# Optimization experiments

Measured on AMD Instinct MI355X. Metric: run time of the kernel, lower is better.

Reference implementation:

```python
import jax, jax.numpy as jnp
import numpy as np

B, S, D, H = 2, 2048, 1024, 16
HD = D // H  # head_dim = 64


def setup_inputs() -> dict:
    key = jax.random.key(0)
    ks = jax.random.split(key, 9)
    s = 1.0 / np.sqrt(D)
    return {
        "x": jax.random.normal(ks[0], (B, S, D), dtype=jnp.float32),
        "Wq": jax.random.uniform(ks[1], (D, D), jnp.float32, -s, s),
        "bq": jnp.zeros((D,), jnp.float32),
        "Wk": jax.random.uniform(ks[2], (D, D), jnp.float32, -s, s),
        "bk": jnp.zeros((D,), jnp.float32),
        "Wv": jax.random.uniform(ks[3], (D, D), jnp.float32, -s, s),
        "bv": jnp.zeros((D,), jnp.float32),
        "Wo": jax.random.uniform(ks[4], (D, D), jnp.float32, -s, s),
        "bo": jnp.zeros((D,), jnp.float32),
    }


def reference(x, Wq, bq, Wk, bk, Wv, bv, Wo, bo):
    # x: [B,S,D] -> Q/K/V: [B,H,S,HD]
    def heads(t):
        return t.reshape(B, S, H, HD).transpose(0, 2, 1, 3)

    Q = heads(x @ Wq + bq)
    K = heads(x @ Wk + bk)
    V = heads(x @ Wv + bv)
    scale = jnp.sqrt(jnp.asarray(HD, dtype=x.dtype))
    energy = jnp.einsum("bhqd,bhkd->bhqk", Q, K) / scale  # [B,H,S,S]
    attn = jax.nn.softmax(energy, axis=-1)
    # dropout is identity in eval mode
    o = jnp.einsum("bhqk,bhkd->bhqd", attn, V)  # [B,H,S,HD]
    o = o.transpose(0, 2, 1, 3).reshape(B, S, D)
    return o @ Wo + bo
```

## Files before the change

### kernel.cpp

```cpp
#include <hip/hip_runtime.h>
#include <hip/hip_bf16.h>

#define B_  2
#define S_  2048
#define D_  1024
#define H_  16
#define HD_ 64

typedef __attribute__((ext_vector_type(8))) short bf16x8;
typedef __attribute__((ext_vector_type(4))) float f32x4;

typedef __attribute__((address_space(1))) const short gbl_short;
typedef __attribute__((address_space(3))) short lds_short;

__device__ __forceinline__ short f2bf(float f) {
  union { float f; unsigned u; } v; v.f = f;
  unsigned r = (v.u + 0x7FFFu + ((v.u >> 16) & 1u)) >> 16;
  return (short)r;
}

__device__ __forceinline__ short bf16s(float f) {
  __hip_bfloat16 h = __float2bfloat16(f);
  return *reinterpret_cast<short*>(&h);
}

__global__ __launch_bounds__(256) void cast_x_kernel(const float* __restrict__ x,
                                                     short* __restrict__ xb) {
  int i = blockIdx.x * 256 + threadIdx.x;
  float4 v = ((const float4*)x)[i];
  short4 o;
  o.x = f2bf(v.x); o.y = f2bf(v.y); o.z = f2bf(v.z); o.w = f2bf(v.w);
  ((short4*)xb)[i] = o;
}

__global__ __launch_bounds__(256) void transpose_cast_w(
    const float* __restrict__ w0, const float* __restrict__ w1,
    const float* __restrict__ w2, const float* __restrict__ w3,
    short* __restrict__ t0, short* __restrict__ t1,
    short* __restrict__ t2, short* __restrict__ t3) {
  const float* W = blockIdx.z == 0 ? w0 : blockIdx.z == 1 ? w1 : blockIdx.z == 2 ? w2 : w3;
  short* T       = blockIdx.z == 0 ? t0 : blockIdx.z == 1 ? t1 : blockIdx.z == 2 ? t2 : t3;
  __shared__ float tile[32][33];
  int tx = threadIdx.x, ty = threadIdx.y;
  int x0 = blockIdx.x * 32, y0 = blockIdx.y * 32;
#pragma unroll
  for (int i = 0; i < 4; ++i)
    tile[ty + i * 8][tx] = W[(y0 + ty + i * 8) * D_ + x0 + tx];
  __syncthreads();
#pragma unroll
  for (int i = 0; i < 4; ++i)
    T[(x0 + ty + i * 8) * D_ + y0 + tx] = f2bf(tile[tx][ty + i * 8]);
}

__device__ __forceinline__ void gemm_mainloop(
    const short* __restrict__ A, const short* __restrict__ Bt, int K,
    int m0, int n0, short* lA, short* lB, f32x4 acc[4][4],
    int lane, int wave) {
  const int l15 = lane & 15, quad = lane >> 4;
  const int wm = wave & 1, wn = wave >> 1;
  const int srow = lane >> 2;
  const int skp  = (lane & 3) * 8;

  for (int kk = 0; kk < K; kk += 32) {
#pragma unroll
    for (int j = 0; j < 2; ++j) {
      int c = wave * 2 + j;
      int row = c * 16 + srow;
      __builtin_amdgcn_global_load_lds(
          (gbl_short*)(A + (m0 + row) * K + kk + skp),
          (lds_short*)(lA + c * 512 + lane * 8), 16, 0, 0);
      __builtin_amdgcn_global_load_lds(
          (gbl_short*)(Bt + (n0 + row) * K + kk + skp),
          (lds_short*)(lB + c * 512 + lane * 8), 16, 0, 0);
    }
    __syncthreads();

    bf16x8 af[4], bf[4];
#pragma unroll
    for (int i = 0; i < 4; ++i) {
      af[i] = *(const bf16x8*)(lA + (wm * 64 + i * 16 + l15) * 32 + quad * 8);
      bf[i] = *(const bf16x8*)(lB + (wn * 64 + i * 16 + l15) * 32 + quad * 8);
    }
#pragma unroll
    for (int mi = 0; mi < 4; ++mi)
#pragma unroll
      for (int ni = 0; ni < 4; ++ni)
        acc[mi][ni] = __builtin_amdgcn_mfma_f32_16x16x32_bf16(af[mi], bf[ni], acc[mi][ni], 0, 0, 0);
    __syncthreads();
  }
}

__global__ __launch_bounds__(256) void qkv_gemm(
    const short* __restrict__ xb,
    const short* __restrict__ Wqt, const short* __restrict__ Wkt, const short* __restrict__ Wvt,
    const float* __restrict__ bq, const float* __restrict__ bk, const float* __restrict__ bv,
    short* __restrict__ Qb, short* __restrict__ Kb, short* __restrict__ Vtb) {
  const int which = blockIdx.z;
  const short* Bt   = which == 0 ? Wqt : which == 1 ? Wkt : Wvt;
  const float* bias = which == 0 ? bq  : which == 1 ? bk  : bv;
  const float scl   = which == 0 ? 0.125f * 1.44269504089f : 1.0f;
  const int lane = threadIdx.x & 63, wave = threadIdx.x >> 6;
  const int l15 = lane & 15, quad = lane >> 4;
  const int wm = wave & 1, wn = wave >> 1;
  const int m0 = blockIdx.x * 128, n0 = blockIdx.y * 128;

  __shared__ short lA[128 * 32];
  __shared__ short lB[128 * 32];

  f32x4 acc[4][4];
#pragma unroll
  for (int mi = 0; mi < 4; ++mi)
#pragma unroll
    for (int ni = 0; ni < 4; ++ni) { f32x4 z = {0.f, 0.f, 0.f, 0.f}; acc[mi][ni] = z; }

  gemm_mainloop(xb, Bt, D_, m0, n0, lA, lB, acc, lane, wave);

#pragma unroll
  for (int mi = 0; mi < 4; ++mi) {
    int m = m0 + wm * 64 + mi * 16 + quad * 4;
    int bb = m >> 11;
    int s0 = m & (S_ - 1);
#pragma unroll
    for (int ni = 0; ni < 4; ++ni) {
      int n = n0 + wn * 64 + ni * 16 + l15;
      int h = n >> 6, hd = n & 63;
      float bsv = bias[n];
      if (which < 2) {
        short* dst = which == 0 ? Qb : Kb;
#pragma unroll
        for (int r = 0; r < 4; ++r)
          dst[((bb * H_ + h) * S_ + (s0 + r)) * HD_ + hd] = f2bf((acc[mi][ni][r] + bsv) * scl);
      } else {
        short4 pk;
        pk.x = f2bf(acc[mi][ni][0] + bsv);
        pk.y = f2bf(acc[mi][ni][1] + bsv);
        pk.z = f2bf(acc[mi][ni][2] + bsv);
        pk.w = f2bf(acc[mi][ni][3] + bsv);
        *(short4*)(Vtb + ((bb * H_ + h) * HD_ + hd) * S_ + s0) = pk;
      }
    }
  }
}

__global__ __launch_bounds__(256) void out_gemm(
    const short* __restrict__ Ob, const short* __restrict__ Wot,
    const float* __restrict__ bo, float* __restrict__ out) {
  const int lane = threadIdx.x & 63, wave = threadIdx.x >> 6;
  const int l15 = lane & 15, quad = lane >> 4;
  const int m0 = blockIdx.x * 128, n0 = blockIdx.y * 64;
  const int srow = lane >> 2;
  const int skp  = (lane & 3) * 8;

  __shared__ short lA[128 * 32];
  __shared__ short lB[64 * 32];

  f32x4 acc[2][4];
#pragma unroll
  for (int mi = 0; mi < 2; ++mi)
#pragma unroll
    for (int ni = 0; ni < 4; ++ni) { f32x4 z = {0.f, 0.f, 0.f, 0.f}; acc[mi][ni] = z; }

  for (int kk = 0; kk < D_; kk += 32) {
#pragma unroll
    for (int j = 0; j < 2; ++j) {
      int c = wave * 2 + j;
      __builtin_amdgcn_global_load_lds(
          (gbl_short*)(Ob + (m0 + c * 16 + srow) * D_ + kk + skp),
          (lds_short*)(lA + c * 512 + lane * 8), 16, 0, 0);
    }
    __builtin_amdgcn_global_load_lds(
        (gbl_short*)(Wot + (n0 + wave * 16 + srow) * D_ + kk + skp),
        (lds_short*)(lB + wave * 512 + lane * 8), 16, 0, 0);
    __syncthreads();

    bf16x8 af[2], bf[4];
#pragma unroll
    for (int i = 0; i < 2; ++i)
      af[i] = *(const bf16x8*)(lA + (wave * 32 + i * 16 + l15) * 32 + quad * 8);
#pragma unroll
    for (int i = 0; i < 4; ++i)
      bf[i] = *(const bf16x8*)(lB + (i * 16 + l15) * 32 + quad * 8);
#pragma unroll
    for (int mi = 0; mi < 2; ++mi)
#pragma unroll
      for (int ni = 0; ni < 4; ++ni)
        acc[mi][ni] = __builtin_amdgcn_mfma_f32_16x16x32_bf16(af[mi], bf[ni], acc[mi][ni], 0, 0, 0);
    __syncthreads();
  }

#pragma unroll
  for (int mi = 0; mi < 2; ++mi) {
    int m = m0 + wave * 32 + mi * 16 + quad * 4;
#pragma unroll
    for (int ni = 0; ni < 4; ++ni) {
      int n = n0 + ni * 16 + l15;
      float bsv = bo[n];
#pragma unroll
      for (int r = 0; r < 4; ++r)
        out[(m + r) * D_ + n] = acc[mi][ni][r] + bsv;
    }
  }
}

__global__ __launch_bounds__(512, 4) void attn_kernel(
    const short* __restrict__ Qb, const short* __restrict__ Kb,
    const short* __restrict__ Vtb, short* __restrict__ Ob) {
  const int qt = blockIdx.x, h = blockIdx.y, b = blockIdx.z;
  const int base = (b * H_ + h) * S_ * HD_;
  const int tid = threadIdx.x;
  const int lane = tid & 63, wave = tid >> 6;
  const int l15 = lane & 15, quad = lane >> 4;

  __shared__ short lK[64 * 64];
  __shared__ short lV[64 * 64];
  __shared__ short lP[8][16 * 88];

  const int q0 = qt * 128 + wave * 16;

  bf16x8 qf[2];
#pragma unroll
  for (int ks = 0; ks < 2; ++ks)
    qf[ks] = *(const bf16x8*)(Qb + base + (q0 + l15) * HD_ + ks * 32 + quad * 8);

  f32x4 oacc[4];
#pragma unroll
  for (int nb = 0; nb < 4; ++nb) { f32x4 z = {0.f, 0.f, 0.f, 0.f}; oacc[nb] = z; }
  f32x4 lacc = {0.f, 0.f, 0.f, 0.f};

  bf16x8 onesf;
#pragma unroll
  for (int i = 0; i < 8; ++i) onesf[i] = (short)0x3F80;

  const int srow = lane >> 3;
  const int sgrp = ((lane & 7) ^ srow) * 8;
  const short* kp = Kb + base + (wave * 8 + srow) * HD_ + sgrp;
  const short* vp = Vtb + base + (wave * 8 + srow) * S_ + sgrp;
  lds_short* ldk = (lds_short*)(lK + wave * 512 + lane * 8);
  lds_short* ldv = (lds_short*)(lV + wave * 512 + lane * 8);

  short* pw = &lP[wave][0];
  const int swz = l15 & 7;

  for (int kt = 0; kt < 32; ++kt) {
    __builtin_amdgcn_global_load_lds((gbl_short*)kp, ldk, 16, 0, 0);
    __builtin_amdgcn_global_load_lds((gbl_short*)vp, ldv, 16, 0, 0);
    kp += 64 * HD_;
    vp += 64;
    __syncthreads();

    f32x4 sacc[4];
#pragma unroll
    for (int nb = 0; nb < 4; ++nb) { f32x4 z = {0.f, 0.f, 0.f, 0.f}; sacc[nb] = z; }
#pragma unroll
    for (int nb = 0; nb < 4; ++nb)
#pragma unroll
      for (int ks = 0; ks < 2; ++ks) {
        bf16x8 kf = *(const bf16x8*)(lK + (nb * 16 + l15) * 64 + (((ks * 4 + quad) ^ swz) * 8));
        sacc[nb] = __builtin_amdgcn_mfma_f32_16x16x32_bf16(qf[ks], kf, sacc[nb], 0, 0, 0);
      }

#pragma unroll
    for (int nb = 0; nb < 4; ++nb)
#pragma unroll
      for (int r = 0; r < 4; ++r)
        pw[(quad * 4 + r) * 88 + nb * 16 + l15] = bf16s(__builtin_amdgcn_exp2f(sacc[nb][r]));

    bf16x8 af[2];
#pragma unroll
    for (int ks = 0; ks < 2; ++ks)
      af[ks] = *(const bf16x8*)(pw + l15 * 88 + ks * 32 + quad * 8);
#pragma unroll
    for (int nbh = 0; nbh < 4; ++nbh)
#pragma unroll
      for (int ks = 0; ks < 2; ++ks) {
        bf16x8 vf = *(const bf16x8*)(lV + (nbh * 16 + l15) * 64 + (((ks * 4 + quad) ^ swz) * 8));
        oacc[nbh] = __builtin_amdgcn_mfma_f32_16x16x32_bf16(af[ks], vf, oacc[nbh], 0, 0, 0);
      }
    lacc = __builtin_amdgcn_mfma_f32_16x16x32_bf16(af[0], onesf, lacc, 0, 0, 0);
    lacc = __builtin_amdgcn_mfma_f32_16x16x32_bf16(af[1], onesf, lacc, 0, 0, 0);
    __syncthreads();
  }

#pragma unroll
  for (int r = 0; r < 4; ++r) {
    float inv = 1.0f / lacc[r];
    int sg = q0 + quad * 4 + r;
#pragma unroll
    for (int nbh = 0; nbh < 4; ++nbh)
      Ob[(b * S_ + sg) * D_ + h * HD_ + nbh * 16 + l15] = bf16s(oacc[nbh][r] * inv);
  }
}

extern "C" void kernel_launch(void* const* d_in, const int* in_sizes, int n_in,
                              void* d_out, int out_size, void* d_ws, size_t ws_size,
                              hipStream_t stream) {
  (void)in_sizes; (void)n_in; (void)out_size; (void)ws_size;
  const float* x  = (const float*)d_in[0];
  const float* Wq = (const float*)d_in[1];
  const float* bq = (const float*)d_in[2];
  const float* Wk = (const float*)d_in[3];
  const float* bk = (const float*)d_in[4];
  const float* Wv = (const float*)d_in[5];
  const float* bv = (const float*)d_in[6];
  const float* Wo = (const float*)d_in[7];
  const float* bo = (const float*)d_in[8];
  float* out = (float*)d_out;

  char* ws = (char*)d_ws;
  short* xb  = (short*)(ws);
  short* Wqt = (short*)(ws + 8388608);
  short* Wkt = Wqt + 1048576;
  short* Wvt = Wkt + 1048576;
  short* Wot = Wvt + 1048576;
  short* Qb  = Wot + 1048576;
  short* Kb  = Qb + 4194304;
  short* Vtb = Kb + 4194304;
  short* Ob  = Vtb + 4194304;

  cast_x_kernel<<<4096, 256, 0, stream>>>(x, xb);
  transpose_cast_w<<<dim3(32, 32, 4), dim3(32, 8), 0, stream>>>(
      Wq, Wk, Wv, Wo, Wqt, Wkt, Wvt, Wot);
  qkv_gemm<<<dim3(32, 8, 3), 256, 0, stream>>>(
      xb, Wqt, Wkt, Wvt, bq, bk, bv, Qb, Kb, Vtb);
  attn_kernel<<<dim3(16, 16, 2), 512, 0, stream>>>(Qb, Kb, Vtb, Ob);
  out_gemm<<<dim3(32, 16), 256, 0, stream>>>(Ob, Wot, bo, out);
}
```

Baseline: 214.0 us.

## Split attention keys across two wave groups and double GEMM k-step

The attention kernel now gives each wave 32 query rows instead of 16, so every K/V fragment read from LDS feeds two MFMAs. The 512 threads are split into two groups that each process half of the key sequence. Their partial outputs and row sums are combined through LDS at the end. The QKV and output GEMMs now stage 64-wide k slices per barrier, which halves the number of loop iterations and syncs. The trade-off is much more LDS per block: the attention kernel's footprint grows to roughly 77KB, which cuts the number of resident blocks. The GEMMs also need more registers and LDS.

```diff
diff --git a/kernel.cpp b/kernel.cpp
--- a/kernel.cpp
+++ b/kernel.cpp
@@ -52,16 +52,16 @@
     T[(x0 + ty + i * 8) * D_ + y0 + tx] = f2bf(tile[tx][ty + i * 8]);
 }
 
-__device__ __forceinline__ void gemm_mainloop(
+__device__ __forceinline__ void gemm_mainloop64(
     const short* __restrict__ A, const short* __restrict__ Bt, int K,
-    int m0, int n0, short* lA, short* lB, f32x4 acc[4][4],
-    int lane, int wave) {
+    int m0, int n0, short* lA, short* lB, short* lA2, short* lB2,
+    f32x4 acc[4][4], int lane, int wave) {
   const int l15 = lane & 15, quad = lane >> 4;
   const int wm = wave & 1, wn = wave >> 1;
   const int srow = lane >> 2;
   const int skp  = (lane & 3) * 8;
 
-  for (int kk = 0; kk < K; kk += 32) {
+  for (int kk = 0; kk < K; kk += 64) {
 #pragma unroll
     for (int j = 0; j < 2; ++j) {
       int c = wave * 2 + j;
@@ -72,20 +72,30 @@
       __builtin_amdgcn_global_load_lds(
           (gbl_short*)(Bt + (n0 + row) * K + kk + skp),
           (lds_short*)(lB + c * 512 + lane * 8), 16, 0, 0);
-    }
-    __syncthreads();
-
-    bf16x8 af[4], bf[4];
+      __builtin_amdgcn_global_load_lds(
+          (gbl_short*)(A + (m0 + row) * K + kk + 32 + skp),
+          (lds_short*)(lA2 + c * 512 + lane * 8), 16, 0, 0);
+      __builtin_amdgcn_global_load_lds(
+          (gbl_short*)(Bt + (n0 + row) * K + kk + 32 + skp),
+          (lds_short*)(lB2 + c * 512 + lane * 8), 16, 0, 0);
+    }
+    __syncthreads();
+
+    bf16x8 af[4], bf[4], af2[4], bf2[4];
 #pragma unroll
     for (int i = 0; i < 4; ++i) {
-      af[i] = *(const bf16x8*)(lA + (wm * 64 + i * 16 + l15) * 32 + quad * 8);
-      bf[i] = *(const bf16x8*)(lB + (wn * 64 + i * 16 + l15) * 32 + quad * 8);
+      af[i]  = *(const bf16x8*)(lA  + (wm * 64 + i * 16 + l15) * 32 + quad * 8);
+      bf[i]  = *(const bf16x8*)(lB  + (wn * 64 + i * 16 + l15) * 32 + quad * 8);
+      af2[i] = *(const bf16x8*)(lA2 + (wm * 64 + i * 16 + l15) * 32 + quad * 8);
+      bf2[i] = *(const bf16x8*)(lB2 + (wn * 64 + i * 16 + l15) * 32 + quad * 8);
     }
 #pragma unroll
     for (int mi = 0; mi < 4; ++mi)
 #pragma unroll
-      for (int ni = 0; ni < 4; ++ni)
-        acc[mi][ni] = __builtin_amdgcn_mfma_f32_16x16x32_bf16(af[mi], bf[ni], acc[mi][ni], 0, 0, 0);
+      for (int ni = 0; ni < 4; ++ni) {
+        acc[mi][ni] = __builtin_amdgcn_mfma_f32_16x16x32_bf16(af[mi],  bf[ni],  acc[mi][ni], 0, 0, 0);
+        acc[mi][ni] = __builtin_amdgcn_mfma_f32_16x16x32_bf16(af2[mi], bf2[ni], acc[mi][ni], 0, 0, 0);
+      }
     __syncthreads();
   }
 }
@@ -106,6 +116,8 @@
 
   __shared__ short lA[128 * 32];
   __shared__ short lB[128 * 32];
+  __shared__ short lA2[128 * 32];
+  __shared__ short lB2[128 * 32];
 
   f32x4 acc[4][4];
 #pragma unroll
@@ -113,7 +125,7 @@
 #pragma unroll
     for (int ni = 0; ni < 4; ++ni) { f32x4 z = {0.f, 0.f, 0.f, 0.f}; acc[mi][ni] = z; }
 
-  gemm_mainloop(xb, Bt, D_, m0, n0, lA, lB, acc, lane, wave);
+  gemm_mainloop64(xb, Bt, D_, m0, n0, lA, lB, lA2, lB2, acc, lane, wave);
 
 #pragma unroll
   for (int mi = 0; mi < 4; ++mi) {
@@ -152,7 +164,9 @@
   const int skp  = (lane & 3) * 8;
 
   __shared__ short lA[128 * 32];
+  __shared__ short lA2[128 * 32];
   __shared__ short lB[64 * 32];
+  __shared__ short lB2[64 * 32];
 
   f32x4 acc[2][4];
 #pragma unroll
@@ -160,31 +174,43 @@
 #pragma unroll
     for (int ni = 0; ni < 4; ++ni) { f32x4 z = {0.f, 0.f, 0.f, 0.f}; acc[mi][ni] = z; }
 
-  for (int kk = 0; kk < D_; kk += 32) {
+  for (int kk = 0; kk < D_; kk += 64) {
 #pragma unroll
     for (int j = 0; j < 2; ++j) {
       int c = wave * 2 + j;
       __builtin_amdgcn_global_load_lds(
           (gbl_short*)(Ob + (m0 + c * 16 + srow) * D_ + kk + skp),
           (lds_short*)(lA + c * 512 + lane * 8), 16, 0, 0);
+      __builtin_amdgcn_global_load_lds(
+          (gbl_short*)(Ob + (m0 + c * 16 + srow) * D_ + kk + 32 + skp),
+          (lds_short*)(lA2 + c * 512 + lane * 8), 16, 0, 0);
     }
     __builtin_amdgcn_global_load_lds(
         (gbl_short*)(Wot + (n0 + wave * 16 + srow) * D_ + kk + skp),
         (lds_short*)(lB + wave * 512 + lane * 8), 16, 0, 0);
-    __syncthreads();
-
-    bf16x8 af[2], bf[4];
-#pragma unroll
-    for (int i = 0; i < 2; ++i)
-      af[i] = *(const bf16x8*)(lA + (wave * 32 + i * 16 + l15) * 32 + quad * 8);
-#pragma unroll
-    for (int i = 0; i < 4; ++i)
-      bf[i] = *(const bf16x8*)(lB + (i * 16 + l15) * 32 + quad * 8);
-#pragma unroll
-    for (int mi = 0; mi < 2; ++mi)
-#pragma unroll
-      for (int ni = 0; ni < 4; ++ni)
-        acc[mi][ni] = __builtin_amdgcn_mfma_f32_16x16x32_bf16(af[mi], bf[ni], acc[mi][ni], 0, 0, 0);
+    __builtin_amdgcn_global_load_lds(
+        (gbl_short*)(Wot + (n0 + wave * 16 + srow) * D_ + kk + 32 + skp),
+        (lds_short*)(lB2 + wave * 512 + lane * 8), 16, 0, 0);
+    __syncthreads();
+
+    bf16x8 af[2], bf[4], af2[2], bf2[4];
+#pragma unroll
+    for (int i = 0; i < 2; ++i) {
+      af[i]  = *(const bf16x8*)(lA  + (wave * 32 + i * 16 + l15) * 32 + quad * 8);
+      af2[i] = *(const bf16x8*)(lA2 + (wave * 32 + i * 16 + l15) * 32 + quad * 8);
+    }
+#pragma unroll
+    for (int i = 0; i < 4; ++i) {
+      bf[i]  = *(const bf16x8*)(lB  + (i * 16 + l15) * 32 + quad * 8);
+      bf2[i] = *(const bf16x8*)(lB2 + (i * 16 + l15) * 32 + quad * 8);
+    }
+#pragma unroll
+    for (int mi = 0; mi < 2; ++mi)
+#pragma unroll
+      for (int ni = 0; ni < 4; ++ni) {
+        acc[mi][ni] = __builtin_amdgcn_mfma_f32_16x16x32_bf16(af[mi],  bf[ni],  acc[mi][ni], 0, 0, 0);
+        acc[mi][ni] = __builtin_amdgcn_mfma_f32_16x16x32_bf16(af2[mi], bf2[ni], acc[mi][ni], 0, 0, 0);
+      }
     __syncthreads();
   }
 
@@ -209,85 +235,139 @@
   const int base = (b * H_ + h) * S_ * HD_;
   const int tid = threadIdx.x;
   const int lane = tid & 63, wave = tid >> 6;
+  const int grp = wave >> 2;
+  const int wq  = wave & 3;
   const int l15 = lane & 15, quad = lane >> 4;
 
-  __shared__ short lK[64 * 64];
-  __shared__ short lV[64 * 64];
-  __shared__ short lP[8][16 * 88];
-
-  const int q0 = qt * 128 + wave * 16;
-
-  bf16x8 qf[2];
-#pragma unroll
-  for (int ks = 0; ks < 2; ++ks)
-    qf[ks] = *(const bf16x8*)(Qb + base + (q0 + l15) * HD_ + ks * 32 + quad * 8);
-
-  f32x4 oacc[4];
-#pragma unroll
-  for (int nb = 0; nb < 4; ++nb) { f32x4 z = {0.f, 0.f, 0.f, 0.f}; oacc[nb] = z; }
-  f32x4 lacc = {0.f, 0.f, 0.f, 0.f};
+  __shared__ __align__(16) short lK[2][64 * 64];
+  __shared__ __align__(16) short lV[2][64 * 64];
+  __shared__ __align__(16) short lP[8][32 * 88];
+
+  const int q0 = qt * 128 + wq * 32;
+
+  bf16x8 qf[2][2];
+#pragma unroll
+  for (int mi = 0; mi < 2; ++mi)
+#pragma unroll
+    for (int ks = 0; ks < 2; ++ks)
+      qf[mi][ks] = *(const bf16x8*)(Qb + base + (q0 + mi * 16 + l15) * HD_ + ks * 32 + quad * 8);
+
+  f32x4 oacc[2][4];
+  f32x4 lacc[2];
+#pragma unroll
+  for (int mi = 0; mi < 2; ++mi) {
+    f32x4 z = {0.f, 0.f, 0.f, 0.f};
+    lacc[mi] = z;
+#pragma unroll
+    for (int nb = 0; nb < 4; ++nb) oacc[mi][nb] = z;
+  }
 
   bf16x8 onesf;
 #pragma unroll
   for (int i = 0; i < 8; ++i) onesf[i] = (short)0x3F80;
 
-  const int srow = lane >> 3;
-  const int sgrp = ((lane & 7) ^ srow) * 8;
-  const short* kp = Kb + base + (wave * 8 + srow) * HD_ + sgrp;
-  const short* vp = Vtb + base + (wave * 8 + srow) * S_ + sgrp;
-  lds_short* ldk = (lds_short*)(lK + wave * 512 + lane * 8);
-  lds_short* ldv = (lds_short*)(lV + wave * 512 + lane * 8);
+  const int tig  = tid & 255;
+  const int slot = tig & 7;
+  const int rbase = tig >> 3;
+  const int sgrp = ((slot ^ (rbase & 7))) * 8;
+  const short* kp = Kb + base + (grp * 1024 + rbase) * HD_ + sgrp;
+  const short* vp = Vtb + base + rbase * S_ + grp * 1024 + sgrp;
+  lds_short* ldk0 = (lds_short*)(&lK[grp][0] + tig * 8);
+  lds_short* ldv0 = (lds_short*)(&lV[grp][0] + tig * 8);
 
   short* pw = &lP[wave][0];
   const int swz = l15 & 7;
 
-  for (int kt = 0; kt < 32; ++kt) {
-    __builtin_amdgcn_global_load_lds((gbl_short*)kp, ldk, 16, 0, 0);
-    __builtin_amdgcn_global_load_lds((gbl_short*)vp, ldv, 16, 0, 0);
+  for (int kt = 0; kt < 16; ++kt) {
+#pragma unroll
+    for (int j = 0; j < 2; ++j) {
+      __builtin_amdgcn_global_load_lds((gbl_short*)(kp + j * 32 * HD_), ldk0 + j * 2048, 16, 0, 0);
+      __builtin_amdgcn_global_load_lds((gbl_short*)(vp + j * 32 * S_),  ldv0 + j * 2048, 16, 0, 0);
+    }
     kp += 64 * HD_;
     vp += 64;
     __syncthreads();
 
-    f32x4 sacc[4];
-#pragma unroll
-    for (int nb = 0; nb < 4; ++nb) { f32x4 z = {0.f, 0.f, 0.f, 0.f}; sacc[nb] = z; }
+    f32x4 sacc[2][4];
+#pragma unroll
+    for (int mi = 0; mi < 2; ++mi)
+#pragma unroll
+      for (int nb = 0; nb < 4; ++nb) { f32x4 z = {0.f, 0.f, 0.f, 0.f}; sacc[mi][nb] = z; }
 #pragma unroll
     for (int nb = 0; nb < 4; ++nb)
 #pragma unroll
       for (int ks = 0; ks < 2; ++ks) {
-        bf16x8 kf = *(const bf16x8*)(lK + (nb * 16 + l15) * 64 + (((ks * 4 + quad) ^ swz) * 8));
-        sacc[nb] = __builtin_amdgcn_mfma_f32_16x16x32_bf16(qf[ks], kf, sacc[nb], 0, 0, 0);
-      }
-
-#pragma unroll
-    for (int nb = 0; nb < 4; ++nb)
-#pragma unroll
-      for (int r = 0; r < 4; ++r)
-        pw[(quad * 4 + r) * 88 + nb * 16 + l15] = bf16s(__builtin_amdgcn_exp2f(sacc[nb][r]));
-
-    bf16x8 af[2];
-#pragma unroll
-    for (int ks = 0; ks < 2; ++ks)
-      af[ks] = *(const bf16x8*)(pw + l15 * 88 + ks * 32 + quad * 8);
+        bf16x8 kf = *(const bf16x8*)(&lK[grp][0] + (nb * 16 + l15) * 64 + (((ks * 4 + quad) ^ swz) * 8));
+        sacc[0][nb] = __builtin_amdgcn_mfma_f32_16x16x32_bf16(qf[0][ks], kf, sacc[0][nb], 0, 0, 0);
+        sacc[1][nb] = __builtin_amdgcn_mfma_f32_16x16x32_bf16(qf[1][ks], kf, sacc[1][nb], 0, 0, 0);
+      }
+
+#pragma unroll
+    for (int mi = 0; mi < 2; ++mi)
+#pragma unroll
+      for (int nb = 0; nb < 4; ++nb)
+#pragma unroll
+        for (int r = 0; r < 4; ++r)
+          pw[(mi * 16 + quad * 4 + r) * 88 + nb * 16 + l15] =
+              bf16s(__builtin_amdgcn_exp2f(sacc[mi][nb][r]));
+
+    bf16x8 af[2][2];
+#pragma unroll
+    for (int mi = 0; mi < 2; ++mi)
+#pragma unroll
+      for (int ks = 0; ks < 2; ++ks)
+        af[mi][ks] = *(const bf16x8*)(pw + (mi * 16 + l15) * 88 + ks * 32 + quad * 8);
 #pragma unroll
     for (int nbh = 0; nbh < 4; ++nbh)
 #pragma unroll
       for (int ks = 0; ks < 2; ++ks) {
-        bf16x8 vf = *(const bf16x8*)(lV + (nbh * 16 + l15) * 64 + (((ks * 4 + quad) ^ swz) * 8));
-        oacc[nbh] = __builtin_amdgcn_mfma_f32_16x16x32_bf16(af[ks], vf, oacc[nbh], 0, 0, 0);
-      }
-    lacc = __builtin_amdgcn_mfma_f32_16x16x32_bf16(af[0], onesf, lacc, 0, 0, 0);
-    lacc = __builtin_amdgcn_mfma_f32_16x16x32_bf16(af[1], onesf, lacc, 0, 0, 0);
-    __syncthreads();
-  }
-
-#pragma unroll
-  for (int r = 0; r < 4; ++r) {
-    float inv = 1.0f / lacc[r];
-    int sg = q0 + quad * 4 + r;
-#pragma unroll
-    for (int nbh = 0; nbh < 4; ++nbh)
-      Ob[(b * S_ + sg) * D_ + h * HD_ + nbh * 16 + l15] = bf16s(oacc[nbh][r] * inv);
+        bf16x8 vf = *(const bf16x8*)(&lV[grp][0] + (nbh * 16 + l15) * 64 + (((ks * 4 + quad) ^ swz) * 8));
+        oacc[0][nbh] = __builtin_amdgcn_mfma_f32_16x16x32_bf16(af[0][ks], vf, oacc[0][nbh], 0, 0, 0);
+        oacc[1][nbh] = __builtin_amdgcn_mfma_f32_16x16x32_bf16(af[1][ks], vf, oacc[1][nbh], 0, 0, 0);
+      }
+#pragma unroll
+    for (int mi = 0; mi < 2; ++mi) {
+      lacc[mi] = __builtin_amdgcn_mfma_f32_16x16x32_bf16(af[mi][0], onesf, lacc[mi], 0, 0, 0);
+      lacc[mi] = __builtin_amdgcn_mfma_f32_16x16x32_bf16(af[mi][1], onesf, lacc[mi], 0, 0, 0);
+    }
+    __syncthreads();
+  }
+
+  float* exch = (float*)(&lP[0][0]);
+  float* lex  = exch + 4 * 2048;
+  if (grp == 1) {
+#pragma unroll
+    for (int mi = 0; mi < 2; ++mi)
+#pragma unroll
+      for (int nbh = 0; nbh < 4; ++nbh)
+#pragma unroll
+        for (int r = 0; r < 4; ++r)
+          exch[wq * 2048 + (mi * 16 + quad * 4 + r) * 64 + nbh * 16 + l15] = oacc[mi][nbh][r];
+    if (l15 == 0) {
+#pragma unroll
+      for (int mi = 0; mi < 2; ++mi)
+#pragma unroll
+        for (int r = 0; r < 4; ++r)
+          lex[wq * 32 + mi * 16 + quad * 4 + r] = lacc[mi][r];
+    }
+  }
+  __syncthreads();
+  if (grp == 0) {
+#pragma unroll
+    for (int mi = 0; mi < 2; ++mi)
+#pragma unroll
+      for (int r = 0; r < 4; ++r) {
+        int row = mi * 16 + quad * 4 + r;
+        float l2 = lex[wq * 32 + row];
+        float inv = 1.0f / (lacc[mi][r] + l2);
+        int sg = q0 + row;
+#pragma unroll
+        for (int nbh = 0; nbh < 4; ++nbh) {
+          float o2 = exch[wq * 2048 + row * 64 + nbh * 16 + l15];
+          Ob[(b * S_ + sg) * D_ + h * HD_ + nbh * 16 + l15] =
+              bf16s((oacc[mi][nbh][r] + o2) * inv);
+        }
+      }
   }
 }
 
```

After: 203.8 us. 4.8% less time.
